# Kernel tuning notes

Hardware: AMD Instinct MI355X
Metric: run time of the kernel (lower is better)

The kernel has to match this reference:

```python
import jax, jax.numpy as jnp
from jax import lax
import numpy as np

NMS_THRESH = 0.5
SCORE_THRESH = 0.05
MAX_DET = 300
B, N, C, P = 8, 20000, 80, 51


def _iou_one_to_many(box, boxes):
    # box: (4,) in (x1,y1,x2,y2); boxes: (N,4). Same IoU math as tf.image.non_max_suppression.
    ix1 = jnp.maximum(box[0], boxes[:, 0])
    iy1 = jnp.maximum(box[1], boxes[:, 1])
    ix2 = jnp.minimum(box[2], boxes[:, 2])
    iy2 = jnp.minimum(box[3], boxes[:, 3])
    inter = jnp.maximum(ix2 - ix1, 0.0) * jnp.maximum(iy2 - iy1, 0.0)
    area_b = (box[2] - box[0]) * (box[3] - box[1])
    area_n = (boxes[:, 2] - boxes[:, 0]) * (boxes[:, 3] - boxes[:, 1])
    union = area_b + area_n - inter
    return jnp.where(union > 0.0, inter / union, 0.0)


def _greedy_nms(boxes, scores):
    """Fixed-length greedy NMS. scores already has -inf at entries below score threshold.
    Returns (idx, keep): idx (MAX_DET,) int32 selected box indices, keep (MAX_DET,) bool validity."""
    bx = lax.stop_gradient(boxes)           # NMS indices are non-differentiable
    s0 = lax.stop_gradient(scores)

    def step(s, _):
        i = jnp.argmax(s)
        ok = s[i] > -jnp.inf
        ious = _iou_one_to_many(bx[i], bx)
        s = jnp.where(ious > NMS_THRESH, -jnp.inf, s)
        s = s.at[i].set(-jnp.inf)
        return s, (i.astype(jnp.int32), ok)

    _, (idx, keep) = lax.scan(step, s0, None, length=MAX_DET)
    return idx, keep


def _filter_one(boxes, classification, relationship):
    # boxes (N,4), classification (N,C), relationship (N,P)
    n_cls = classification.shape[1]
    masked = jnp.where(classification > SCORE_THRESH, classification, -jnp.inf)  # (N,C)
    per_cls = masked.T                                                            # (C,N)

    # class-specific NMS, vectorized over classes
    idx, keep = jax.vmap(lambda s: _greedy_nms(boxes, s))(per_cls)  # (C,MAX_DET) each

    cand = jnp.take_along_axis(per_cls, idx.astype(jnp.int32), axis=1)  # (C,MAX_DET)
    cand = jnp.where(keep, cand, -jnp.inf)

    flat = cand.reshape(-1)                        # (C*MAX_DET,)
    top_s, top_pos = lax.top_k(flat, MAX_DET)      # global top-k over all classes
    box_idx = idx.reshape(-1)[top_pos]             # (MAX_DET,)
    label = top_pos // MAX_DET                     # class id (flatten order (C,M))
    valid = jnp.isfinite(top_s)

    out_boxes = jnp.where(valid[:, None], boxes[box_idx], -1.0)              # (MAX_DET,4)
    out_scores = jnp.where(valid, top_s, -1.0)                               # (MAX_DET,)
    out_labels = jnp.where(valid, label, -1).astype(jnp.int32)

    pred = relationship[box_idx]                                             # (MAX_DET,P)
    pred_labels = jnp.where(valid, jnp.argmax(pred, axis=1), -1).astype(jnp.int32)
    pred_scores = jnp.where(valid, jnp.max(pred, axis=1), -1.0)
    return out_boxes, out_scores, out_labels, pred_scores, pred_labels


def setup_inputs() -> dict:
    key = jax.random.key(0)
    k1, k2, k3, k4 = jax.random.split(key, 4)
    xy = jax.random.uniform(k1, (B, N, 2), dtype=jnp.float32) * 700.0
    wh = jax.random.uniform(k2, (B, N, 2), dtype=jnp.float32) * 100.0 + 1.0
    boxes = jnp.concatenate([xy, xy + wh], axis=-1)                   # valid (x1,y1,x2,y2)
    classification = jax.random.uniform(k3, (B, N, C), dtype=jnp.float32)
    relationship = jax.random.uniform(k4, (B, N, P), dtype=jnp.float32)
    return {"boxes": boxes, "classification": classification, "relationship": relationship}


def reference(boxes, classification, relationship):
    return jax.vmap(_filter_one)(boxes, classification, relationship)
```

## Files before the change

### kernel.cpp

```cpp
#include <hip/hip_runtime.h>
#include <hip/hip_bf16.h>
#include <math.h>

#define NBATCH 8
#define NBOX   20000
#define NCLS   80
#define NREL   51
#define MAXDET 300
#define NTOT   (NCLS * MAXDET)
#define CAP    512
#define SPECCAP 2560
#define NHB    3328
#define HB0    (0x3F666666u >> 9)
#define TARGETK 480u
#define SCORE_THR 0.05f
#define SPEC_THRF 0.9f
#define WWAVES 8

typedef unsigned long long u64;
typedef unsigned int u32;

__device__ __forceinline__ bool iou_sup(float ax1, float ay1, float ax2, float ay2, float aarea,
                                        float bx1, float by1, float bx2, float by2, float barea) {
  float ix1 = fmaxf(ax1, bx1);
  float iy1 = fmaxf(ay1, by1);
  float ix2 = fminf(ax2, bx2);
  float iy2 = fminf(ay2, by2);
  float dw = fmaxf(__fsub_rn(ix2, ix1), 0.0f);
  float dh = fmaxf(__fsub_rn(iy2, iy1), 0.0f);
  float inter = __fmul_rn(dw, dh);
  float uni = __fsub_rn(__fadd_rn(aarea, barea), inter);
  if (!(uni > 0.0f)) return false;
  return __fdiv_rn(inter, uni) > 0.5f;
}

__device__ __forceinline__ bool iou_gt_half(float ax1, float ay1, float ax2, float ay2,
                                            float bx1, float by1, float bx2, float by2) {
  float aa = __fmul_rn(__fsub_rn(ax2, ax1), __fsub_rn(ay2, ay1));
  float ab = __fmul_rn(__fsub_rn(bx2, bx1), __fsub_rn(by2, by1));
  return iou_sup(ax1, ay1, ax2, ay2, aa, bx1, by1, bx2, by2, ab);
}

__device__ __forceinline__ bool iou_sup_fast(float ax1, float ay1, float ax2, float ay2,
                                             float aarea, float bx1, float by1, float bx2,
                                             float by2, float barea) {
  float ix1 = fmaxf(ax1, bx1);
  float iy1 = fmaxf(ay1, by1);
  float ix2 = fminf(ax2, bx2);
  float iy2 = fminf(ay2, by2);
  float dw = fmaxf(__fsub_rn(ix2, ix1), 0.0f);
  float dh = fmaxf(__fsub_rn(iy2, iy1), 0.0f);
  float inter = __fmul_rn(dw, dh);
  float uni = __fsub_rn(__fadd_rn(aarea, barea), inter);
  return (uni > 0.0f) && (inter > __fmul_rn(0.5f, uni));
}

#define CEXR(x, y, asc) { bool sw_ = (asc) ? ((x) > (y)) : ((x) < (y)); \
                          if (sw_) { u64 t_ = (x); (x) = (y); (y) = t_; } }

__device__ __forceinline__ void bitonic_sort(u64* keys, int SZ, int tid) {
  for (int k = 2; k <= SZ; k <<= 1) {
    for (int j = k >> 1; j >= 4; j >>= 1) {
      for (int v = tid; v < (SZ >> 1); v += 256) {
        int i = ((v & ~(j - 1)) << 1) | (v & (j - 1));
        int p = i | j;
        bool asc = ((i & k) == 0);
        u64 a = keys[i], b = keys[p];
        bool sw = asc ? (a > b) : (a < b);
        if (sw) { keys[i] = b; keys[p] = a; }
      }
      __syncthreads();
    }
    if (tid < (SZ >> 2)) {
      ulonglong2* k2 = (ulonglong2*)keys;
      ulonglong2 lo = k2[tid * 2], hi = k2[tid * 2 + 1];
      u64 a = lo.x, b = lo.y, c = hi.x, d = hi.y;
      int i0 = tid << 2;
      if (k == 2) {
        CEXR(a, b, true); CEXR(c, d, false);
      } else {
        bool asc = ((i0 & k) == 0);
        CEXR(a, c, asc); CEXR(b, d, asc);
        CEXR(a, b, asc); CEXR(c, d, asc);
      }
      lo.x = a; lo.y = b; hi.x = c; hi.y = d;
      k2[tid * 2] = lo; k2[tid * 2 + 1] = hi;
    }
    __syncthreads();
  }
}

template <int NB>
__device__ __forceinline__ void suffix_fast(const u32* hist, u32 cap, u32* wsum4, u32* sout) {
  const int tid = threadIdx.x, lane = tid & 63, w = tid >> 6;
  const int G = NB / 256;
  u32 v = 0;
  const int hb = tid * G;
#pragma unroll
  for (int t = 0; t < G; ++t) v += hist[hb + t];
  u32 s = v;
#pragma unroll
  for (int off = 1; off < 64; off <<= 1) {
    u32 t2 = __shfl_down(s, off);
    if (lane + off < 64) s += t2;
  }
  if (lane == 0) wsum4[w] = s;
  __syncthreads();
  u32 total = wsum4[0] + wsum4[1] + wsum4[2] + wsum4[3];
  u32 after = 0;
#pragma unroll
  for (int ww = 1; ww < 4; ++ww) if (ww > w) after += wsum4[ww];
  u32 inc = s + after;
  u32 exc = inc - v;
  if (tid == 0) {
    sout[3] = total;
    if (total == 0u) { sout[0] = 0u; sout[1] = 0u; sout[2] = 0u; }
  }
  u32 target = total < cap ? total : cap;
  if (total != 0u && inc >= target && exc < target) {
    u32 acc = exc;
    for (int u = hb + G - 1; u >= hb; --u) {
      acc += hist[u];
      if (acc >= target) { sout[0] = (u32)u; sout[1] = acc; sout[2] = acc - hist[u]; break; }
    }
  }
  __syncthreads();
}

__global__ __launch_bounds__(256) void k_tr(const float* __restrict__ cls,
                                            float* __restrict__ colS,
                                            u32* __restrict__ ghist,
                                            u32* __restrict__ gtail) {
  __shared__ float tile[NCLS * 65];
  const int tid = threadIdx.x;
  const int b = blockIdx.y;
  const int n0 = blockIdx.x * 64;
  if (blockIdx.x == 0) {
    for (int i = tid; i < NHB; i += 256) ghist[b * NHB + i] = 0u;
    if (tid == 0) gtail[b] = 0u;
  }
  const int rows = (NBOX - n0) < 64 ? (NBOX - n0) : 64;
  const float4* src4 = (const float4*)(cls + ((size_t)b * NBOX + n0) * NCLS);
  const int nq = rows * (NCLS / 4);
  for (int i = tid; i < nq; i += 256) {
    int rr = i / (NCLS / 4);
    int c4 = i - rr * (NCLS / 4);
    float4 v = src4[i];
    tile[(c4 * 4 + 0) * 65 + rr] = v.x;
    tile[(c4 * 4 + 1) * 65 + rr] = v.y;
    tile[(c4 * 4 + 2) * 65 + rr] = v.z;
    tile[(c4 * 4 + 3) * 65 + rr] = v.w;
  }
  __syncthreads();
  float4* dst4 = (float4*)colS;
  for (int i = tid; i < NCLS * 16; i += 256) {
    int c = i >> 4, nl = i & 15;
    if (nl * 4 < rows) {
      float4 v;
      v.x = tile[c * 65 + nl * 4 + 0];
      v.y = tile[c * 65 + nl * 4 + 1];
      v.z = tile[c * 65 + nl * 4 + 2];
      v.w = tile[c * 65 + nl * 4 + 3];
      dst4[(((size_t)b * NCLS + c) * NBOX + n0) / 4 + nl] = v;
    }
  }
}

__global__ __launch_bounds__(256) void k_zero(u32* __restrict__ ghist,
                                              u32* __restrict__ gtail) {
  const int b = blockIdx.x;
  const int tid = threadIdx.x;
  for (int i = tid; i < NHB; i += 256) ghist[b * NHB + i] = 0u;
  if (tid == 0) gtail[b] = 0u;
}

template <int STRIDE>
__device__ __forceinline__ float4 load4s(const float* col, int q) {
  if (STRIDE == 1) return ((const float4*)col)[q];
  float4 v;
  v.x = col[(size_t)(q * 4 + 0) * STRIDE];
  v.y = col[(size_t)(q * 4 + 1) * STRIDE];
  v.z = col[(size_t)(q * 4 + 2) * STRIDE];
  v.w = col[(size_t)(q * 4 + 3) * STRIDE];
  return v;
}

template <int STRIDE>
__global__ __launch_bounds__(256) void k_sel(const float* __restrict__ scores,
                                             u64* __restrict__ keysBase, size_t kstride,
                                             int* __restrict__ selCnt,
                                             int* __restrict__ totCnt,
                                             int* __restrict__ flags) {
  __shared__ __align__(16) char smem[SPECCAP * 8 + NHB * 4 + CAP * 8];
  u64* side = (u64*)smem;
  u32* hist = (u32*)(smem + SPECCAP * 8);
  u64* keys = (u64*)(smem + SPECCAP * 8 + NHB * 4);
  __shared__ u32 wsum[4], selB[4], twave[4];
  __shared__ u32 s_scnt, s_cnt;

  const int tid = threadIdx.x;
  const int lane = tid & 63;
  const int w = tid >> 6;
  const u64 lmask = (1ull << lane) - 1ull;
  const int bc = blockIdx.x;
  const int b = bc / NCLS, c = bc % NCLS;
  const float* col = (STRIDE == 1) ? (scores + (size_t)bc * NBOX)
                                   : (scores + (size_t)b * NBOX * NCLS + c);

  for (int i = tid; i < NHB; i += 256) hist[i] = 0u;
  if (tid == 0) { s_scnt = 0u; s_cnt = 0u; }
  __syncthreads();

  u32 tailc = 0;
  for (int base = 0; base < NBOX / 4; base += 2048) {
    float4 v[8];
#pragma unroll
    for (int p = 0; p < 8; ++p) {
      int q = base + tid + (p << 8);
      if (q < NBOX / 4) v[p] = load4s<STRIDE>(col, q);
    }
#pragma unroll
    for (int p = 0; p < 8; ++p) {
      int q = base + tid + (p << 8);
      if (q < NBOX / 4) {
        float vv[4] = {v[p].x, v[p].y, v[p].z, v[p].w};
#pragma unroll
        for (int e = 0; e < 4; ++e) {
          float s = vv[e];
          bool spec = s > SPEC_THRF;
          if (s > SCORE_THR && !spec) ++tailc;
          u64 mb = __ballot(spec);
          if (mb) {
            u32 bs;
            if (lane == 0) bs = atomicAdd(&s_scnt, (u32)__popcll(mb));
            bs = __shfl(bs, 0);
            if (spec) {
              u32 bits = __float_as_uint(s);
              u32 pos = bs + (u32)__popcll(mb & lmask);
              if (pos < SPECCAP) side[pos] = ((u64)bits << 32) | (~(u32)(q * 4 + e));
              u32 h = (bits >> 9) - HB0;
              if (h > NHB - 1) h = NHB - 1;
              atomicAdd(&hist[h], 1u);
            }
          }
        }
      }
    }
  }
  u32 tr = tailc;
#pragma unroll
  for (int off = 1; off < 64; off <<= 1) tr += __shfl_down(tr, off);
  if (lane == 0) twave[w] = tr;
  __syncthreads();

  const u32 specCount = s_scnt;
  const u32 tailSum = twave[0] + twave[1] + twave[2] + twave[3];
  const u32 totalAll = specCount + tailSum;

  if (totalAll == 0u) {
    if (tid == 0) { selCnt[bc] = 0; totCnt[bc] = 0; flags[bc] = 0; }
    return;
  }
  const u32 target = totalAll < TARGETK ? totalAll : TARGETK;
  if (specCount < target || specCount > SPECCAP) {
    if (tid == 0) { selCnt[bc] = 0; totCnt[bc] = (int)totalAll; flags[bc] = 1; }
    return;
  }

  suffix_fast<NHB>(hist, target, wsum, selB);
  const u32 F0 = selB[0];
  const u32 selCount = selB[1];
  if (selCount > CAP) {
    if (tid == 0) { selCnt[bc] = 0; totCnt[bc] = (int)totalAll; flags[bc] = 1; }
    return;
  }

  const int iters = (int)((specCount + 255u) >> 8);
  for (int it2 = 0; it2 < iters; ++it2) {
    u32 idx = (u32)it2 * 256u + (u32)tid;
    bool act = idx < specCount;
    u64 key = act ? side[idx] : 0ull;
    u32 bits = (u32)(key >> 32);
    u32 h = (bits >> 9) - HB0;
    if (h > NHB - 1) h = NHB - 1;
    bool sel = act && (h >= F0);
    u64 ms = __ballot(sel);
    if (ms) {
      u32 bs;
      if (lane == 0) bs = atomicAdd(&s_cnt, (u32)__popcll(ms));
      bs = __shfl(bs, 0);
      if (sel) keys[bs + (u32)__popcll(ms & lmask)] = key;
    }
  }
  __syncthreads();
  for (int i = (int)selCount + tid; i < CAP; i += 256) keys[i] = 0ull;
  __syncthreads();

  bitonic_sort(keys, CAP, tid);

  u64* kout = keysBase + (size_t)bc * kstride;
  for (int i = tid; i < CAP; i += 256) kout[i] = keys[i];
  if (tid == 0) { selCnt[bc] = (int)selCount; totCnt[bc] = (int)totalAll; flags[bc] = 0; }
}

__global__ __launch_bounds__(512) void k_walk(const float* __restrict__ boxes,
                                              const u64* __restrict__ keysBase, size_t kstride,
                                              const int* __restrict__ selCnt,
                                              const int* __restrict__ totCnt,
                                              float* __restrict__ keptScore,
                                              int* __restrict__ keptN,
                                              int* __restrict__ keptCount,
                                              int* __restrict__ flags,
                                              u32* __restrict__ ghist,
                                              u32* __restrict__ gtail) {
  __shared__ u64 keys[CAP];
  __shared__ float4 candbox[CAP];
  __shared__ float carea[CAP];
  __shared__ float4 keptbox[MAXDET];
  __shared__ float karea[MAXDET];
  __shared__ int kn[MAXDET];
  __shared__ float ksc[MAXDET];
  __shared__ u64 supW[WWAVES];
  __shared__ u64 mpart[WWAVES][64];
  __shared__ int s_kept;

  const int tid = threadIdx.x;
  const int lane = tid & 63;
  const int w = tid >> 6;
  const u64 lmask = (1ull << lane) - 1ull;
  const int bc = blockIdx.x;
  const int b = bc / NCLS;

  if (flags[bc] != 0) return;
  const u32 selCount = (u32)selCnt[bc];
  const u32 totalAll = (u32)totCnt[bc];

  const u64* kin = keysBase + (size_t)bc * kstride;
  for (int i = tid; i < CAP; i += 512) keys[i] = kin[i];
  if (tid == 0) s_kept = 0;
  __syncthreads();

  for (int i = tid; i < (int)selCount; i += 512) {
    int pos = CAP - 1 - i;
    u32 n = ~((u32)keys[pos]);
    float4 bb = ((const float4*)boxes)[(size_t)b * NBOX + n];
    candbox[pos] = bb;
    carea[pos] = __fmul_rn(__fsub_rn(bb.z, bb.x), __fsub_rn(bb.w, bb.y));
  }
  __syncthreads();

  const u32 ntile = (selCount + 63u) >> 6;
  for (u32 t = 0; t < ntile; ++t) {
    const int kept0 = s_kept;
    if (kept0 >= MAXDET) break;
    const u32 r = t * 64u + (u32)lane;
    const bool valid = r < selCount;
    const int si = valid ? (CAP - 1 - (int)r) : (CAP - 1);
    float4 mybox = candbox[si];
    float marea = carea[si];
    bool sup = false;
    for (int k = w; k < kept0; k += WWAVES) {
      float4 kb = keptbox[k];
      if (iou_sup_fast(kb.x, kb.y, kb.z, kb.w, karea[k],
                       mybox.x, mybox.y, mybox.z, mybox.w, marea))
        sup = true;
    }
    u64 bal = __ballot(sup);
    if (lane == 0) supW[w] = bal;
    u64 mw = 0ull;
    const int ebase = w * 8;
#pragma unroll
    for (int ee = 0; ee < 8; ++ee) {
      const int e = ebase + ee;
      int ei = CAP - 1 - (int)(t * 64u) - e;
      float4 eb = candbox[ei];
      if (e < lane && iou_sup_fast(eb.x, eb.y, eb.z, eb.w, carea[ei],
                                   mybox.x, mybox.y, mybox.z, mybox.w, marea))
        mw |= 1ull << e;
    }
    mpart[w][lane] = mw;
    __syncthreads();
    if (w == 0) {
      u64 prior = 0ull, m = 0ull;
#pragma unroll
      for (int ww = 0; ww < WWAVES; ++ww) {
        prior |= supW[ww];
        m |= mpart[ww][lane];
      }
      u64 remaining = __ballot(valid) & ~prior;
      u64 keptmask = 0ull;
      const int room = MAXDET - kept0;
      while (remaining != 0ull && (int)__popcll(keptmask) < room) {
        int j = __ffsll((long long)remaining) - 1;
        keptmask |= 1ull << j;
        remaining &= ~(1ull << j);
        u64 supj = __ballot(((m >> j) & 1ull) != 0ull);
        remaining &= ~supj;
      }
      if ((keptmask >> lane) & 1ull) {
        int pos = kept0 + (int)__popcll(keptmask & lmask);
        u64 mykey = keys[CAP - 1 - (int)r];
        keptbox[pos] = mybox;
        karea[pos] = marea;
        kn[pos] = (int)(~((u32)mykey));
        ksc[pos] = __uint_as_float((u32)(mykey >> 32));
      }
      if (lane == 0) s_kept = kept0 + (int)__popcll(keptmask);
    }
    __syncthreads();
  }

  const int kept = s_kept;
  const bool exhausted = (kept < MAXDET && selCount < totalAll);
  for (int rr = tid; rr < MAXDET; rr += 512) {
    keptScore[bc * MAXDET + rr] = (rr < kept) ? ksc[rr] : -INFINITY;
    keptN[bc * MAXDET + rr] = (rr < kept) ? kn[rr] : 0;
  }
  if (tid == 0) {
    keptCount[bc] = kept;
    flags[bc] = exhausted ? 1 : 0;
  }
  if (!exhausted) {
    for (int rr = tid; rr < kept; rr += 512) {
      float s = ksc[rr];
      if (s > SPEC_THRF) {
        u32 h = (__float_as_uint(s) >> 9) - HB0;
        if (h > NHB - 1) h = NHB - 1;
        atomicAdd(&ghist[b * NHB + h], 1u);
      } else {
        atomicAdd(&gtail[b], 1u);
      }
    }
  }
}

__global__ __launch_bounds__(256) void k_slow(const float* __restrict__ boxes,
                                              const float* __restrict__ cls,
                                              float* __restrict__ keptScore,
                                              int* __restrict__ keptN,
                                              int* __restrict__ keptCount,
                                              const int* __restrict__ flags,
                                              u32* __restrict__ ghist,
                                              u32* __restrict__ gtail) {
  const int bc = blockIdx.x;
  if (flags[bc] != 1) return;
  const int tid = threadIdx.x;
  const int b = bc / NCLS, c = bc % NCLS;
  const float* col = cls + (size_t)b * NBOX * NCLS + c;
  __shared__ u32 sup[(NBOX + 31) / 32];
  __shared__ u64 red[256];
  __shared__ float4 sbx;
  __shared__ int s_kept;
  for (int i = tid; i < (NBOX + 31) / 32; i += 256) sup[i] = 0u;
  if (tid == 0) s_kept = 0;
  __syncthreads();
  for (int it = 0; it < MAXDET; ++it) {
    u64 best = 0ull;
    for (int n = tid; n < NBOX; n += 256) {
      if ((sup[n >> 5] >> (n & 31)) & 1u) continue;
      float s = col[(size_t)n * NCLS];
      if (s > SCORE_THR) {
        u64 key = ((u64)__float_as_uint(s) << 32) | (~(u32)n);
        if (key > best) best = key;
      }
    }
    red[tid] = best;
    __syncthreads();
    for (int off = 128; off > 0; off >>= 1) {
      if (tid < off) { u64 o = red[tid + off]; if (o > red[tid]) red[tid] = o; }
      __syncthreads();
    }
    u64 win = red[0];
    if (win == 0ull) break;
    u32 nw = ~((u32)win);
    if (tid == 0) {
      int k = s_kept;
      keptScore[bc * MAXDET + k] = __uint_as_float((u32)(win >> 32));
      keptN[bc * MAXDET + k] = (int)nw;
      s_kept = k + 1;
      sbx = ((const float4*)boxes)[(size_t)b * NBOX + nw];
    }
    __syncthreads();
    float4 bx = sbx;
    for (int n = tid; n < NBOX; n += 256) {
      float4 cb = ((const float4*)boxes)[(size_t)b * NBOX + n];
      if (iou_gt_half(bx.x, bx.y, bx.z, bx.w, cb.x, cb.y, cb.z, cb.w))
        atomicOr(&sup[n >> 5], 1u << (n & 31));
    }
    if (tid == 0) atomicOr(&sup[nw >> 5], 1u << (nw & 31));
    __syncthreads();
  }
  __syncthreads();
  const int kept = s_kept;
  for (int r = kept + tid; r < MAXDET; r += 256) {
    keptScore[bc * MAXDET + r] = -INFINITY;
    keptN[bc * MAXDET + r] = 0;
  }
  for (int rr = tid; rr < kept; rr += 256) {
    float s = keptScore[bc * MAXDET + rr];
    if (s > SPEC_THRF) {
      u32 h = (__float_as_uint(s) >> 9) - HB0;
      if (h > NHB - 1) h = NHB - 1;
      atomicAdd(&ghist[b * NHB + h], 1u);
    } else {
      atomicAdd(&gtail[b], 1u);
    }
  }
  if (tid == 0) keptCount[bc] = kept;
}

__global__ __launch_bounds__(256) void k_osort(const float* __restrict__ boxes,
                                               const float* __restrict__ rel,
                                               const float* __restrict__ keptScore,
                                               const int* __restrict__ keptN,
                                               const u32* __restrict__ ghist,
                                               const u32* __restrict__ gtail,
                                               float* __restrict__ out) {
  __shared__ u64 keys[1024];
  __shared__ u32 wsum[4], selB[4];
  __shared__ u32 s_cnt;
  const int tid = threadIdx.x;
  const int lane = tid & 63;
  const u64 lmask = (1ull << lane) - 1ull;
  const int b = blockIdx.x;
  const float4* ks4 = (const float4*)(keptScore + (size_t)b * NTOT);

  if (tid == 0) s_cnt = 0u;
  suffix_fast<NHB>(ghist + (size_t)b * NHB, (u32)MAXDET, wsum, selB);
  const u32 specTotal = selB[3];
  const u32 totalAll = specTotal + gtail[b];
  const u32 target = totalAll < (u32)MAXDET ? totalAll : (u32)MAXDET;
  const u32 F0 = selB[0];
  const u32 selSpec = selB[1];
  const bool fast = (totalAll != 0u) && (specTotal >= target) && (selSpec <= (u32)CAP);
  int SZ = CAP;

  if (totalAll != 0u) {
    if (fast) {
      for (int base = 0; base < NTOT / 4; base += 2048) {
        float4 v[8];
#pragma unroll
        for (int p = 0; p < 8; ++p) {
          int q = base + tid + (p << 8);
          if (q < NTOT / 4) v[p] = ks4[q];
        }
#pragma unroll
        for (int p = 0; p < 8; ++p) {
          int q = base + tid + (p << 8);
          if (q < NTOT / 4) {
            float vv[4] = {v[p].x, v[p].y, v[p].z, v[p].w};
#pragma unroll
            for (int e = 0; e < 4; ++e) {
              float s = vv[e];
              bool sel = false;
              u32 bits = 0;
              if (s > SPEC_THRF) {
                bits = __float_as_uint(s);
                u32 h = (bits >> 9) - HB0;
                if (h > NHB - 1) h = NHB - 1;
                sel = (h >= F0);
              }
              u64 ms = __ballot(sel);
              if (ms) {
                u32 bs;
                if (lane == 0) bs = atomicAdd(&s_cnt, (u32)__popcll(ms));
                bs = __shfl(bs, 0);
                if (sel)
                  keys[bs + (u32)__popcll(ms & lmask)] =
                      ((u64)bits << 32) | (~(u32)(q * 4 + e));
              }
            }
          }
        }
      }
      __syncthreads();
      for (int i = (int)selSpec + tid; i < CAP; i += 256) keys[i] = 0ull;
      __syncthreads();
      bitonic_sort(keys, CAP, tid);
      SZ = CAP;
    } else {
      if (tid < 64) {
        const int c0 = lane, c1 = 64 + lane;
        const bool has1 = (c1 < NCLS);
        const float* ls0 = keptScore + ((size_t)b * NCLS + c0) * MAXDET;
        const float* ls1 = keptScore + ((size_t)b * NCLS + (has1 ? c1 : c0)) * MAXDET;
        int h0 = 0, h1 = 0;
        float v0 = ls0[0], w0v = ls0[1];
        float v1 = has1 ? ls1[0] : -INFINITY;
        float w1v = has1 ? ls1[1] : -INFINITY;
        for (int r = 0; r < (int)target; ++r) {
          float bs; int bcl;
          if (has1 && v1 > v0) { bs = v1; bcl = c1; } else { bs = v0; bcl = c0; }
#pragma unroll
          for (int off = 32; off > 0; off >>= 1) {
            float os = __shfl_xor(bs, off);
            int oc = __shfl_xor(bcl, off);
            if (os > bs || (os == bs && oc < bcl)) { bs = os; bcl = oc; }
          }
          if (bcl == c0) {
            keys[1023 - r] = ((u64)__float_as_uint(bs) << 32) | (~(u32)(c0 * MAXDET + h0));
            ++h0; v0 = w0v; w0v = (h0 + 1 < MAXDET) ? ls0[h0 + 1] : -INFINITY;
          } else if (has1 && bcl == c1) {
            keys[1023 - r] = ((u64)__float_as_uint(bs) << 32) | (~(u32)(c1 * MAXDET + h1));
            ++h1; v1 = w1v; w1v = (h1 + 1 < MAXDET) ? ls1[h1 + 1] : -INFINITY;
          }
        }
      }
      __syncthreads();
      SZ = 1024;
    }
  }

  for (int r = tid; r < MAXDET; r += 256) {
    const bool valid = (u32)r < target;
    float s = -1.0f, pm = -1.0f, pl = -1.0f, cl = -1.0f;
    float4 ob; ob.x = ob.y = ob.z = ob.w = -1.0f;
    if (valid) {
      u64 key = keys[SZ - 1 - r];
      u32 fp = ~((u32)key);
      int c = (int)(fp / MAXDET);
      int slot = (int)(fp - (u32)c * MAXDET);
      int n = keptN[((size_t)b * NCLS + c) * MAXDET + slot];
      s = __uint_as_float((u32)(key >> 32));
      cl = (float)c;
      size_t nb = (size_t)b * NBOX + (u32)n;
      ob = ((const float4*)boxes)[nb];
      const float* rp = rel + nb * NREL;
      float vr[NREL];
#pragma unroll
      for (int p = 0; p < NREL; ++p) vr[p] = rp[p];
      float best = vr[0]; int bi = 0;
#pragma unroll
      for (int p = 1; p < NREL; ++p) { if (vr[p] > best) { best = vr[p]; bi = p; } }
      pm = best; pl = (float)bi;
    }
    ((float4*)out)[(size_t)b * MAXDET + r] = ob;
    const int sbase = NBATCH * MAXDET * 4;
    out[sbase + b * MAXDET + r] = s;
    out[sbase + NBATCH * MAXDET + b * MAXDET + r] = cl;
    out[sbase + 2 * NBATCH * MAXDET + b * MAXDET + r] = pm;
    out[sbase + 3 * NBATCH * MAXDET + b * MAXDET + r] = pl;
  }
}

extern "C" void kernel_launch(void* const* d_in, const int* in_sizes, int n_in,
                              void* d_out, int out_size, void* d_ws, size_t ws_size,
                              hipStream_t stream) {
  (void)in_sizes; (void)n_in; (void)out_size;
  const float* boxes = (const float*)d_in[0];
  const float* cls   = (const float*)d_in[1];
  const float* rel   = (const float*)d_in[2];
  float* out = (float*)d_out;
  char* ws = (char*)d_ws;

  const size_t trBytes = (size_t)NBATCH * NCLS * NBOX * 4;
  const size_t NP = NBATCH * NCLS;

  float* colS = (float*)ws;
  size_t off = 0;
  const size_t oKeptScore = off; off += NP * MAXDET * 4;
  const size_t oKeptN     = off; off += NP * MAXDET * 4;
  const size_t oKeptCount = off; off += NP * 4;
  const size_t oFlags     = off; off += NP * 4;
  const size_t oSelCnt    = off; off += NP * 4;
  const size_t oTotCnt    = off; off += NP * 4;
  const size_t oKeysSep   = off; off += NP * CAP * 8;
  const size_t oGhist     = off; off += (size_t)NBATCH * NHB * 4;
  const size_t oGtail     = off; off += NBATCH * 4;
  const size_t kbaseBytes = off;

  const bool useTr = ws_size >= trBytes + kbaseBytes;
  char* kbase = useTr ? (ws + trBytes) : ws;

  float* keptScore = (float*)(kbase + oKeptScore);
  int* keptN = (int*)(kbase + oKeptN);
  int* keptCount = (int*)(kbase + oKeptCount);
  int* flags = (int*)(kbase + oFlags);
  int* selCnt = (int*)(kbase + oSelCnt);
  int* totCnt = (int*)(kbase + oTotCnt);
  u64* keysSep = (u64*)(kbase + oKeysSep);
  u32* ghist = (u32*)(kbase + oGhist);
  u32* gtail = (u32*)(kbase + oGtail);

  u64* keysBase = useTr ? (u64*)colS : keysSep;
  const size_t kstride = useTr ? (size_t)(NBOX / 2) : (size_t)CAP;

  if (useTr) {
    k_tr<<<dim3((NBOX + 63) / 64, NBATCH), 256, 0, stream>>>(cls, colS, ghist, gtail);
    k_sel<1><<<NP, 256, 0, stream>>>(colS, keysBase, kstride, selCnt, totCnt, flags);
  } else {
    k_zero<<<NBATCH, 256, 0, stream>>>(ghist, gtail);
    k_sel<NCLS><<<NP, 256, 0, stream>>>(cls, keysBase, kstride, selCnt, totCnt, flags);
  }
  k_walk<<<NP, 512, 0, stream>>>(boxes, keysBase, kstride, selCnt, totCnt,
                                 keptScore, keptN, keptCount, flags, ghist, gtail);
  k_slow<<<NP, 256, 0, stream>>>(boxes, cls, keptScore, keptN, keptCount, flags,
                                 ghist, gtail);
  k_osort<<<NBATCH, 256, 0, stream>>>(boxes, rel, keptScore, keptN, ghist, gtail, out);
}
```

Before: 142.0 us.

## Precompute pairwise suppression bitmask matrix in k_walk, then single-wave greedy walk

Replaces the tile-by-tile NMS walk in k_walk with a two-phase scheme. First, all 512 threads compute a full lower-triangular suppression bitmask (colM), one 64-bit word per candidate per 64-candidate block. Then a single wavefront walks the tiles, using the kept masks held in registers and AND-ing them with the precomputed columns instead of recomputing IoU against every kept box. This removes the per-tile __syncthreads and the repeated IoU work against the growing kept list, at the cost of computing all O(CAP^2) pairs up front, even when the walk would stop early.

```diff
diff --git a/kernel.cpp b/kernel.cpp
--- a/kernel.cpp
+++ b/kernel.cpp
@@ -15,7 +15,6 @@
 #define TARGETK 480u
 #define SCORE_THR 0.05f
 #define SPEC_THRF 0.9f
-#define WWAVES 8
 
 typedef unsigned long long u64;
 typedef unsigned int u32;
@@ -313,15 +312,12 @@
                                               int* __restrict__ flags,
                                               u32* __restrict__ ghist,
                                               u32* __restrict__ gtail) {
-  __shared__ u64 keys[CAP];
-  __shared__ float4 candbox[CAP];
-  __shared__ float carea[CAP];
-  __shared__ float4 keptbox[MAXDET];
-  __shared__ float karea[MAXDET];
-  __shared__ int kn[MAXDET];
-  __shared__ float ksc[MAXDET];
-  __shared__ u64 supW[WWAVES];
-  __shared__ u64 mpart[WWAVES][64];
+  __shared__ __align__(16) char smem[47104];
+  u64* keys = (u64*)smem;
+  float4* candbox = (float4*)(smem + 4096);
+  float* carea = (float*)(smem + 12288);
+  u64* colM = (u64*)(smem + 14336);
+  __shared__ unsigned short keptIdx[MAXDET];
   __shared__ int s_kept;
 
   const int tid = threadIdx.x;
@@ -341,55 +337,55 @@
   __syncthreads();
 
   for (int i = tid; i < (int)selCount; i += 512) {
-    int pos = CAP - 1 - i;
-    u32 n = ~((u32)keys[pos]);
+    u32 n = ~((u32)keys[CAP - 1 - i]);
     float4 bb = ((const float4*)boxes)[(size_t)b * NBOX + n];
-    candbox[pos] = bb;
-    carea[pos] = __fmul_rn(__fsub_rn(bb.z, bb.x), __fsub_rn(bb.w, bb.y));
-  }
-  __syncthreads();
-
-  const u32 ntile = (selCount + 63u) >> 6;
-  for (u32 t = 0; t < ntile; ++t) {
-    const int kept0 = s_kept;
-    if (kept0 >= MAXDET) break;
-    const u32 r = t * 64u + (u32)lane;
-    const bool valid = r < selCount;
-    const int si = valid ? (CAP - 1 - (int)r) : (CAP - 1);
-    float4 mybox = candbox[si];
-    float marea = carea[si];
-    bool sup = false;
-    for (int k = w; k < kept0; k += WWAVES) {
-      float4 kb = keptbox[k];
-      if (iou_sup_fast(kb.x, kb.y, kb.z, kb.w, karea[k],
-                       mybox.x, mybox.y, mybox.z, mybox.w, marea))
-        sup = true;
-    }
-    u64 bal = __ballot(sup);
-    if (lane == 0) supW[w] = bal;
-    u64 mw = 0ull;
-    const int ebase = w * 8;
-#pragma unroll
-    for (int ee = 0; ee < 8; ++ee) {
-      const int e = ebase + ee;
-      int ei = CAP - 1 - (int)(t * 64u) - e;
-      float4 eb = candbox[ei];
-      if (e < lane && iou_sup_fast(eb.x, eb.y, eb.z, eb.w, carea[ei],
-                                   mybox.x, mybox.y, mybox.z, mybox.w, marea))
-        mw |= 1ull << e;
-    }
-    mpart[w][lane] = mw;
-    __syncthreads();
-    if (w == 0) {
-      u64 prior = 0ull, m = 0ull;
-#pragma unroll
-      for (int ww = 0; ww < WWAVES; ++ww) {
-        prior |= supW[ww];
-        m |= mpart[ww][lane];
-      }
-      u64 remaining = __ballot(valid) & ~prior;
+    candbox[i] = bb;
+    carea[i] = __fmul_rn(__fsub_rn(bb.z, bb.x), __fsub_rn(bb.w, bb.y));
+  }
+  __syncthreads();
+
+  for (int task = tid; task < CAP * 8; task += 512) {
+    int c = task & (CAP - 1);
+    int wd = task >> 9;
+    u64 bits = 0ull;
+    if (c < (int)selCount) {
+      int jmax = c - (wd << 6);
+      if (jmax > 64) jmax = 64;
+      if (jmax > 0) {
+        float4 myb = candbox[c];
+        float ma = carea[c];
+        for (int jj = 0; jj < 64; ++jj) {
+          if (jj < jmax) {
+            int i = (wd << 6) + jj;
+            float4 ib = candbox[i];
+            if (iou_sup_fast(ib.x, ib.y, ib.z, ib.w, carea[i],
+                             myb.x, myb.y, myb.z, myb.w, ma))
+              bits |= 1ull << jj;
+          }
+        }
+      }
+    }
+    colM[c * 8 + wd] = bits;
+  }
+  __syncthreads();
+
+  if (w == 0) {
+    u64 Kreg = 0ull;
+    int kept = 0;
+    const u32 ntile = (selCount + 63u) >> 6;
+    for (u32 t = 0; t < ntile && kept < MAXDET; ++t) {
+      const int c = (int)(t * 64u) + lane;
+      const bool valid = c < (int)selCount;
+      const u64* myCol = &colM[c * 8];
+      u64 prior = 0ull;
+      for (int wd = 0; wd < (int)t; ++wd) {
+        u64 kw = __shfl(Kreg, wd);
+        prior |= myCol[wd] & kw;
+      }
+      u64 m = myCol[t];
+      u64 remaining = __ballot(valid && prior == 0ull);
       u64 keptmask = 0ull;
-      const int room = MAXDET - kept0;
+      const int room = MAXDET - kept;
       while (remaining != 0ull && (int)__popcll(keptmask) < room) {
         int j = __ffsll((long long)remaining) - 1;
         keptmask |= 1ull << j;
@@ -397,24 +393,27 @@
         u64 supj = __ballot(((m >> j) & 1ull) != 0ull);
         remaining &= ~supj;
       }
-      if ((keptmask >> lane) & 1ull) {
-        int pos = kept0 + (int)__popcll(keptmask & lmask);
-        u64 mykey = keys[CAP - 1 - (int)r];
-        keptbox[pos] = mybox;
-        karea[pos] = marea;
-        kn[pos] = (int)(~((u32)mykey));
-        ksc[pos] = __uint_as_float((u32)(mykey >> 32));
-      }
-      if (lane == 0) s_kept = kept0 + (int)__popcll(keptmask);
-    }
-    __syncthreads();
-  }
+      if ((keptmask >> lane) & 1ull)
+        keptIdx[kept + (int)__popcll(keptmask & lmask)] = (unsigned short)c;
+      kept += (int)__popcll(keptmask);
+      if (lane == (int)t) Kreg |= keptmask;
+    }
+    if (lane == 0) s_kept = kept;
+  }
+  __syncthreads();
 
   const int kept = s_kept;
   const bool exhausted = (kept < MAXDET && selCount < totalAll);
   for (int rr = tid; rr < MAXDET; rr += 512) {
-    keptScore[bc * MAXDET + rr] = (rr < kept) ? ksc[rr] : -INFINITY;
-    keptN[bc * MAXDET + rr] = (rr < kept) ? kn[rr] : 0;
+    float sc = -INFINITY;
+    int n = 0;
+    if (rr < kept) {
+      u64 key = keys[CAP - 1 - (int)keptIdx[rr]];
+      sc = __uint_as_float((u32)(key >> 32));
+      n = (int)(~((u32)key));
+    }
+    keptScore[bc * MAXDET + rr] = sc;
+    keptN[bc * MAXDET + rr] = n;
   }
   if (tid == 0) {
     keptCount[bc] = kept;
@@ -422,7 +421,7 @@
   }
   if (!exhausted) {
     for (int rr = tid; rr < kept; rr += 512) {
-      float s = ksc[rr];
+      float s = __uint_as_float((u32)(keys[CAP - 1 - (int)keptIdx[rr]] >> 32));
       if (s > SPEC_THRF) {
         u32 h = (__float_as_uint(s) >> 9) - HB0;
         if (h > NHB - 1) h = NHB - 1;
```

New measurement: 191.3 us. 1.35x slower.
